# Performance work log

Measured on AMD Instinct MI355X. Metric: run time of the kernel, lower is better.

The kernel has to match this reference:

```python
import jax, jax.numpy as jnp
import numpy as np

B, T, D, H = 128, 512, 64, 512  # batch, seq_len, feature dim, hidden dim
S_MIN, S_FRAC = 0.5, 0.5        # aug_args for generate_samp_mask


def setup_inputs() -> dict:
    key = jax.random.key(0)
    ks = jax.random.split(key, 8)
    x = jax.random.normal(ks[0], (B, T, D), jnp.float32)
    # monotonically increasing irregular timestamps
    tp = jnp.cumsum(jax.random.uniform(ks[1], (B, T), jnp.float32, 1e-3, 0.1), axis=1)
    # Deterministic replay of generate_samp_mask: mask[i]=1 -> teacher forcing
    rng = np.random.default_rng(0)
    extrap_ind = int(rng.integers(int(T * S_MIN), T))
    samp_inds = np.sort(rng.choice(np.arange(extrap_ind), int(S_FRAC * extrap_ind), replace=False))
    mask = np.zeros(T, dtype=np.int32)
    mask[samp_inds] = 1
    samp_mask = jnp.asarray(mask)
    s = 1.0 / np.sqrt(H)  # torch GRUCell/Linear default uniform init scale
    W_ih = jax.random.uniform(ks[2], (3 * H, D + 1), jnp.float32, -s, s)
    W_hh = jax.random.uniform(ks[3], (3 * H, H), jnp.float32, -s, s)
    b_ih = jax.random.uniform(ks[4], (3 * H,), jnp.float32, -s, s)
    b_hh = jax.random.uniform(ks[5], (3 * H,), jnp.float32, -s, s)
    W_out = jax.random.uniform(ks[6], (H, D), jnp.float32, -s, s)
    b_out = jax.random.uniform(ks[7], (D,), jnp.float32, -s, s)
    return {"x": x, "tp": tp, "samp_mask": samp_mask, "W_ih": W_ih, "W_hh": W_hh,
            "b_ih": b_ih, "b_hh": b_hh, "W_out": W_out, "b_out": b_out}


def _gru_cell(inp, h, W_ih, W_hh, b_ih, b_hh):
    gi = inp @ W_ih.T + b_ih          # (B, 3H)
    gh = h @ W_hh.T + b_hh            # (B, 3H)
    i_r, i_z, i_n = jnp.split(gi, 3, axis=-1)
    h_r, h_z, h_n = jnp.split(gh, 3, axis=-1)
    r = jax.nn.sigmoid(i_r + h_r)
    z = jax.nn.sigmoid(i_z + h_z)
    n = jnp.tanh(i_n + r * h_n)
    return (1.0 - z) * n + z * h


def reference(x, tp, samp_mask, W_ih, W_hh, b_ih, b_hh, W_out, b_out):
    # delta_t: append time deltas as an extra channel
    offset = jnp.concatenate([jnp.zeros((tp.shape[0], 1), tp.dtype), tp[:, :-1]], axis=1)
    delta = (tp - offset)[..., None]            # (B, T, 1)
    xin = jnp.concatenate([x, delta], axis=-1)  # (B, T, D+1)

    def step(h, inputs):
        x_t, m = inputs                          # (B, D+1), scalar bool
        prev_out = h @ W_out + b_out             # (B, D)
        ar_in = jnp.concatenate([prev_out, x_t[:, -2:-1]], axis=-1)  # (B, D+1)
        inp = jnp.where(m, x_t, ar_in)
        h_new = _gru_cell(inp, h, W_ih, W_hh, b_ih, b_hh)
        return h_new, h_new

    h0 = jnp.zeros((x.shape[0], H), x.dtype)
    _, h_arr = jax.lax.scan(step, h0, (jnp.swapaxes(xin, 0, 1), samp_mask.astype(bool)))
    h_arr = jnp.swapaxes(h_arr, 0, 1)            # (B, T, H)
    out = h_arr @ W_out + b_out                  # (B, T, D)
    # select_by_length with lens == T for every sample -> flat (B*T, D)
    return out.reshape(-1, out.shape[-1])
```

## Files before the change

### kernel.cpp

```cpp
#include <hip/hip_runtime.h>
#include <math.h>

#define TB 512

typedef __attribute__((ext_vector_type(8))) short bf16x8;
typedef __attribute__((ext_vector_type(4))) float f32x4;
typedef unsigned long long u64;

#define FBASE  24576
#define PREP_F (FBASE)
#define XPRE_F (FBASE + 2112)
#define ORED_F (FBASE + 2904)
#define WOC_F  (FBASE + 3448)
#define WIH_F  (FBASE + 3960)
#define SB_F   (FBASE + 5544)
#define XLAST_F (FBASE + 5640)
#define MSK_F  (FBASE + 5672)
#define LDS_FLOATS (FBASE + 6184)
#define LDS_BYTES (LDS_FLOATS * 4)

#define STEP_BYTES 262144
#define GRP_BYTES  65536
#define HIST_NEEDED (4096ull + 513ull * STEP_BYTES)
#define FB_NEEDED   (4096ull + 2ull * STEP_BYTES)

__device__ __forceinline__ unsigned rne16(float f) {
  unsigned u = __float_as_uint(f);
  return (u + 0x7FFFu + ((u >> 16) & 1u)) >> 16;
}
__device__ __forceinline__ float bfhilo(unsigned hh, unsigned hl) {
  return __uint_as_float(hh << 16) + __uint_as_float(hl << 16);
}

__global__ __launch_bounds__(TB, 2) void gru_persistent(
    const float* __restrict__ x, const float* __restrict__ tp, const int* __restrict__ mask,
    const float* __restrict__ W_ih, const float* __restrict__ W_hh,
    const float* __restrict__ b_ih, const float* __restrict__ b_hh,
    const float* __restrict__ W_out, const float* __restrict__ b_out,
    char* __restrict__ data, unsigned* __restrict__ flags,
    float* __restrict__ out, int hmode)
{
  extern __shared__ char smem[];
  float* LP = (float*)smem;
  int* MSK = (int*)&LP[MSK_F];
  const int tid = threadIdx.x;
  const int wg  = blockIdx.x;
  const int s   = wg & 63;
  const int g   = wg >> 6;
  const int bg0 = g * 32;
  const int j0  = 8 * s;
  const int lane = tid & 63;
  const int wv   = tid >> 6;
  const int myct = wv >> 1, mykh = wv & 1;

  MSK[tid] = mask[tid];
  if (tid < 65) {
    for (int p = 0; p < 24; ++p) {
      int row = (p < 8) ? (j0 + p) : (p < 16) ? (512 + j0 + (p - 8)) : (1024 + j0 + (p - 16));
      LP[WIH_F + p * 66 + tid] = W_ih[(size_t)row * 65 + tid];
    }
  }
  LP[WOC_F + tid] = W_out[(size_t)tid * 64 + s];
  if (tid < 16) {
    int row = (tid < 8) ? (j0 + tid) : (512 + j0 + (tid - 8));
    const float* wi = W_ih + (size_t)row * 65;
    float bt = b_ih[row] + b_hh[row];
    float bp = 0.f;
    for (int d = 0; d < 64; ++d) bp = fmaf(wi[d], b_out[d], bp);
    LP[SB_F + tid]      = bt;
    LP[SB_F + 16 + tid] = bt + bp;
    LP[SB_F + 32 + tid] = wi[64];
  } else if (tid < 24) {
    int jj = tid - 16;
    int row = 1024 + j0 + jj;
    const float* wi = W_ih + (size_t)row * 65;
    float bp = 0.f;
    for (int d = 0; d < 64; ++d) bp = fmaf(wi[d], b_out[d], bp);
    LP[SB_F + 48 + jj] = b_hh[row];
    LP[SB_F + 56 + jj] = b_ih[row];
    LP[SB_F + 64 + jj] = b_ih[row] + bp;
    LP[SB_F + 72 + jj] = wi[64];
  }
  if (tid == 0) LP[SB_F + 80] = b_out[s];
  if (tid < 64) {
    u64* p = (u64*)(data + (size_t)g * GRP_BYTES + (size_t)s * 1024 + tid * 16);
    __hip_atomic_store(p,     0ull, __ATOMIC_RELAXED, __HIP_MEMORY_SCOPE_AGENT);
    __hip_atomic_store(p + 1, 0ull, __ATOMIC_RELAXED, __HIP_MEMORY_SCOPE_AGENT);
  }
  __syncthreads();

  {
    const int k = tid;
    const float* wo = W_out + (size_t)k * 64;
    unsigned short* bw16 = (unsigned short*)smem;
    for (int rr = 0; rr < 48; ++rr) {
      int c, col; float w;
      if (rr < 16) {
        c = 1; col = rr;
        int row = (rr < 8) ? (j0 + rr) : (512 + j0 + rr - 8);
        w = W_hh[(size_t)row * 512 + k];
      } else if (rr < 24) {
        c = 0; col = rr - 16;
        w = W_hh[(size_t)(1024 + j0 + rr - 16) * 512 + k];
      } else {
        int p, whrow;
        if (rr < 32) { c = 0; col = rr - 24 + 8; p = 16 + (rr - 24); whrow = -1; }
        else if (rr < 40) { c = 2; col = rr - 32; p = rr - 32; whrow = j0 + rr - 32; }
        else { c = 2; col = rr - 40 + 8; p = 8 + (rr - 40); whrow = 512 + j0 + rr - 40; }
        const float* wr = &LP[WIH_F + p * 66];
        float a = 0.f;
#pragma unroll 8
        for (int d = 0; d < 64; ++d) a = fmaf(wr[d], wo[d], a);
        w = a + (whrow >= 0 ? W_hh[(size_t)whrow * 512 + k] : 0.f);
      }
      unsigned wh = rne16(w);
      float resid = w - __uint_as_float(wh << 16);
      unsigned wl = rne16(resid);
      int base = c * 32768 + (k >> 5) * 1024 + (col | (((k >> 3) & 3) << 4)) * 16 + (k & 7) * 2;
      bw16[base >> 1] = (unsigned short)wh;
      bw16[(base + 16384) >> 1] = (unsigned short)wl;
    }
  }
  __syncthreads();

  bf16x8 Bh[8], Bl[8];
  if (wv < 6) {
#pragma unroll
    for (int i = 0; i < 8; ++i) {
      Bh[i] = *(const bf16x8*)(smem + myct * 32768 + (mykh * 8 + i) * 1024 + lane * 16);
      Bl[i] = *(const bf16x8*)(smem + myct * 32768 + 16384 + (mykh * 8 + i) * 1024 + lane * 16);
    }
  }

  auto stage_x = [&](int tt) {
    if (tt >= 512) return;
    if (MSK[tt] != 0) {
      for (int task = tid; task < 768; task += TB) {
        const int xr = task >> 5, b = task & 31;
        const float* wrow = &LP[WIH_F + xr * 66];
        size_t ti = (size_t)(bg0 + b) * 512 + tt;
        float del = tp[ti] - (tt > 0 ? tp[ti - 1] : 0.f);
        float xa = wrow[64] * del;
        const float4* x4 = (const float4*)(x + ti * 64);
#pragma unroll
        for (int d4 = 0; d4 < 16; ++d4) {
          float4 xv = x4[d4];
          xa = fmaf(wrow[d4 * 4 + 0], xv.x, xa);
          xa = fmaf(wrow[d4 * 4 + 1], xv.y, xa);
          xa = fmaf(wrow[d4 * 4 + 2], xv.z, xa);
          xa = fmaf(wrow[d4 * 4 + 3], xv.w, xa);
        }
        LP[XPRE_F + xr * 33 + b] = xa;
      }
    } else if (tid < 32) {
      LP[XLAST_F + tid] = x[((size_t)(bg0 + tid) * 512 + tt) * 64 + 63];
    }
  };

  stage_x(0);

  unsigned* myflags = &flags[g * 64];

  asm volatile("s_waitcnt vmcnt(0)" ::: "memory");
  __syncthreads();
  if (tid == 0)
    __hip_atomic_store(&myflags[s], 1u, __ATOMIC_RELAXED, __HIP_MEMORY_SCOPE_AGENT);
  if (wv == 0) {
    int cnt = 0;
    while (true) {
      unsigned v = __hip_atomic_load(&myflags[lane], __ATOMIC_RELAXED, __HIP_MEMORY_SCOPE_AGENT);
      if (__ballot(v < 1u) == 0ull) break;
      __builtin_amdgcn_s_sleep(1);
      if (++cnt > 500000) break;
    }
  }
  __syncthreads();

  const unsigned short* ah16 = (const unsigned short*)smem;

  for (int t = 0; t <= 512; ++t) {
    const bool last = (t == 512);
    const bool teacher = (!last) && (MSK[t] != 0);
    const int csel = teacher ? 1 : 2;

    const char* src = data + (size_t)(hmode ? t : (t & 1)) * STEP_BYTES + (size_t)g * GRP_BYTES;
    uint4 v0[4], v1[4];
    if (hmode) {
#pragma unroll
      for (int i = 0; i < 4; ++i) {
        int c = i * 512 + tid, sg = c >> 6, ln = c & 63;
        v0[i] = *(const uint4*)(src + (size_t)((sg * 2 + 0) * 64 + ln) * 16);
        v1[i] = *(const uint4*)(src + (size_t)((sg * 2 + 1) * 64 + ln) * 16);
      }
    } else {
#pragma unroll
      for (int i = 0; i < 4; ++i) {
        int c = i * 512 + tid, sg = c >> 6, ln = c & 63;
        const u64* p0 = (const u64*)(src + (size_t)((sg * 2 + 0) * 64 + ln) * 16);
        const u64* p1 = (const u64*)(src + (size_t)((sg * 2 + 1) * 64 + ln) * 16);
        u64 a0 = __hip_atomic_load(p0,     __ATOMIC_RELAXED, __HIP_MEMORY_SCOPE_AGENT);
        u64 a1 = __hip_atomic_load(p0 + 1, __ATOMIC_RELAXED, __HIP_MEMORY_SCOPE_AGENT);
        u64 b0 = __hip_atomic_load(p1,     __ATOMIC_RELAXED, __HIP_MEMORY_SCOPE_AGENT);
        u64 b1 = __hip_atomic_load(p1 + 1, __ATOMIC_RELAXED, __HIP_MEMORY_SCOPE_AGENT);
        v0[i] = uint4{(unsigned)a0, (unsigned)(a0 >> 32), (unsigned)a1, (unsigned)(a1 >> 32)};
        v1[i] = uint4{(unsigned)b0, (unsigned)(b0 >> 32), (unsigned)b1, (unsigned)(b1 >> 32)};
      }
    }
#pragma unroll
    for (int i = 0; i < 4; ++i) {
      int c = i * 512 + tid, sg = c >> 6, ln = c & 63;
      *(uint4*)(smem + (size_t)(sg * 1024) + ln * 16)        = v0[i];
      *(uint4*)(smem + (size_t)((32 + sg) * 1024) + ln * 16) = v1[i];
    }
    __syncthreads();

    float hp = 0.f;
    if (tid < 256) {
      const int b = tid & 31, jj = tid >> 5;
      const int ks = s >> 2, half = b >> 4;
      const int ln = (b & 15) | ((s & 3) << 4);
      unsigned hh = ah16[((half * 32 + ks) * 1024 + ln * 16 + jj * 2) >> 1];
      unsigned hl = ah16[((half * 32 + 16 + ks) * 1024 + ln * 16 + jj * 2) >> 1];
      hp = bfhilo(hh, hl);
    }

    if (!last && wv < 6 && (myct == 0 || myct == csel)) {
#pragma unroll
      for (int half = 0; half < 2; ++half) {
        f32x4 acc0 = {0.f, 0.f, 0.f, 0.f};
        f32x4 acc1 = {0.f, 0.f, 0.f, 0.f};
        f32x4 acc2 = {0.f, 0.f, 0.f, 0.f};
        f32x4 acc3 = {0.f, 0.f, 0.f, 0.f};
#pragma unroll
        for (int i = 0; i < 8; ++i) {
          const char* abh = smem + (size_t)((half * 32 + mykh * 8 + i) * 1024) + lane * 16;
          bf16x8 ahh = *(const bf16x8*)abh;
          bf16x8 ahl = *(const bf16x8*)(abh + 16 * 1024);
          f32x4& acc = ((i & 3) == 0) ? acc0 : ((i & 3) == 1) ? acc1 : ((i & 3) == 2) ? acc2 : acc3;
          acc = __builtin_amdgcn_mfma_f32_16x16x32_bf16(ahh, Bh[i], acc, 0, 0, 0);
          acc = __builtin_amdgcn_mfma_f32_16x16x32_bf16(ahh, Bl[i], acc, 0, 0, 0);
          acc = __builtin_amdgcn_mfma_f32_16x16x32_bf16(ahl, Bh[i], acc, 0, 0, 0);
        }
        f32x4 acc = (acc0 + acc1) + (acc2 + acc3);
        const int prow = (myct == 0 ? 16 : 0) + (lane & 15);
        const int pcol = half * 16 + ((lane >> 4) << 2);
#pragma unroll
        for (int q = 0; q < 4; ++q)
          LP[PREP_F + mykh * 1056 + prow * 33 + pcol + q] = acc[q];
      }
    }

    if (wv >= 6) {
#pragma unroll
      for (int tk = 0; tk < 4; ++tk) {
        const int task = (tid - 384) + tk * 128;
        const int half = task >> 8, rem = task & 255;
        const int bl = rem & 15, ks = rem >> 4;
        const int b = half * 16 + bl;
        const float* woc = &LP[WOC_F];
        float oa = 0.f;
#pragma unroll
        for (int c = 0; c < 4; ++c) {
          const uint4 wh = *(const uint4*)(smem + (size_t)((half * 32 + ks) * 1024) + (bl | (c << 4)) * 16);
          const uint4 wl = *(const uint4*)(smem + (size_t)((half * 32 + 16 + ks) * 1024) + (bl | (c << 4)) * 16);
          int k0 = ks * 32 + c * 8;
          oa = fmaf(bfhilo(wh.x & 0xFFFFu, wl.x & 0xFFFFu), woc[k0 + 0], oa);
          oa = fmaf(bfhilo(wh.x >> 16, wl.x >> 16), woc[k0 + 1], oa);
          oa = fmaf(bfhilo(wh.y & 0xFFFFu, wl.y & 0xFFFFu), woc[k0 + 2], oa);
          oa = fmaf(bfhilo(wh.y >> 16, wl.y >> 16), woc[k0 + 3], oa);
          oa = fmaf(bfhilo(wh.z & 0xFFFFu, wl.z & 0xFFFFu), woc[k0 + 4], oa);
          oa = fmaf(bfhilo(wh.z >> 16, wl.z >> 16), woc[k0 + 5], oa);
          oa = fmaf(bfhilo(wh.w & 0xFFFFu, wl.w & 0xFFFFu), woc[k0 + 6], oa);
          oa = fmaf(bfhilo(wh.w >> 16, wl.w >> 16), woc[k0 + 7], oa);
        }
        LP[ORED_F + b * 17 + ks] = oa;
      }
    }
    __syncthreads();

    if (!last) {
      if (tid < 256) {
        const int b = tid & 31, jj = tid >> 5;
        float pr  = LP[PREP_F + jj * 33 + b]        + LP[PREP_F + 1056 + jj * 33 + b];
        float pz  = LP[PREP_F + (8 + jj) * 33 + b]  + LP[PREP_F + 1056 + (8 + jj) * 33 + b];
        float pnh = LP[PREP_F + (16 + jj) * 33 + b] + LP[PREP_F + 1056 + (16 + jj) * 33 + b]
                  + LP[SB_F + 48 + jj];
        float pni;
        if (teacher) {
          pr += LP[XPRE_F + jj * 33 + b] + LP[SB_F + jj];
          pz += LP[XPRE_F + (8 + jj) * 33 + b] + LP[SB_F + 8 + jj];
          pni = LP[XPRE_F + (16 + jj) * 33 + b] + LP[SB_F + 56 + jj];
        } else {
          float xl = LP[XLAST_F + b];
          pr += LP[SB_F + 16 + jj] + LP[SB_F + 32 + jj] * xl;
          pz += LP[SB_F + 24 + jj] + LP[SB_F + 40 + jj] * xl;
          pni = LP[PREP_F + (24 + jj) * 33 + b] + LP[PREP_F + 1056 + (24 + jj) * 33 + b]
              + LP[SB_F + 64 + jj] + LP[SB_F + 72 + jj] * xl;
        }
        float rg = 1.f / (1.f + expf(-pr));
        float zg = 1.f / (1.f + expf(-pz));
        float ng = tanhf(fmaf(rg, pnh, pni));
        float hv = fmaf(zg, hp - ng, ng);
        float hvp = __shfl_xor(hv, 32, 64);
        if ((jj & 1) == 0) {
          unsigned h0h = rne16(hv), h1h = rne16(hvp);
          float r0 = hv  - __uint_as_float(h0h << 16);
          float r1 = hvp - __uint_as_float(h1h << 16);
          unsigned hw = h0h | (h1h << 16);
          unsigned lw = rne16(r0) | (rne16(r1) << 16);
          char* dst = data + (size_t)(hmode ? (t + 1) : ((t + 1) & 1)) * STEP_BYTES
                    + (size_t)g * GRP_BYTES;
          const int half = b >> 4, ln2 = (b & 15) | ((s & 3) << 4), ks2 = s >> 2;
          unsigned* dhh = (unsigned*)(dst + (size_t)((ks2 * 2 + half) * 64 + ln2) * 16 + jj * 2);
          unsigned* dhl = (unsigned*)(dst + (size_t)(((16 + ks2) * 2 + half) * 64 + ln2) * 16 + jj * 2);
          __hip_atomic_store(dhh, hw, __ATOMIC_RELAXED, __HIP_MEMORY_SCOPE_AGENT);
          __hip_atomic_store(dhl, lw, __ATOMIC_RELAXED, __HIP_MEMORY_SCOPE_AGENT);
        }
      }
      asm volatile("s_waitcnt vmcnt(0)" ::: "memory");
      __syncthreads();
      const unsigned tgt = (unsigned)(t + 2);
      if (tid == 0)
        __hip_atomic_store(&myflags[s], tgt, __ATOMIC_RELAXED, __HIP_MEMORY_SCOPE_AGENT);
      if (t >= 1 && tid >= 256 && tid < 288) {
        const int b = tid - 256;
        float o = LP[SB_F + 80];
#pragma unroll
        for (int i = 0; i < 16; ++i) o += LP[ORED_F + b * 17 + i];
        out[((size_t)(bg0 + b) * 512 + (t - 1)) * 64 + s] = o;
      }
      stage_x(t + 1);
      if (wv == 0) {
        int cnt = 0;
        while (true) {
          unsigned v = __hip_atomic_load(&myflags[lane], __ATOMIC_RELAXED, __HIP_MEMORY_SCOPE_AGENT);
          if (__ballot(v < tgt) == 0ull) break;
          __builtin_amdgcn_s_sleep(1);
          if (++cnt > 200000) break;
        }
      }
      __syncthreads();
    } else {
      if (tid >= 256 && tid < 288) {
        const int b = tid - 256;
        float o = LP[SB_F + 80];
#pragma unroll
        for (int i = 0; i < 16; ++i) o += LP[ORED_F + b * 17 + i];
        out[((size_t)(bg0 + b) * 512 + 511) * 64 + s] = o;
      }
    }
  }
}

extern "C" void kernel_launch(void* const* d_in, const int* in_sizes, int n_in,
                              void* d_out, int out_size, void* d_ws, size_t ws_size,
                              hipStream_t stream) {
  (void)in_sizes; (void)n_in; (void)out_size;
  const float* x    = (const float*)d_in[0];
  const float* tp   = (const float*)d_in[1];
  const int*   mask = (const int*)d_in[2];
  const float* W_ih = (const float*)d_in[3];
  const float* W_hh = (const float*)d_in[4];
  const float* b_ih = (const float*)d_in[5];
  const float* b_hh = (const float*)d_in[6];
  const float* W_out= (const float*)d_in[7];
  const float* b_out= (const float*)d_in[8];
  float* out = (float*)d_out;
  if (ws_size < FB_NEEDED) return;
  int hmode = (ws_size >= HIST_NEEDED) ? 1 : 0;
  unsigned* flags = (unsigned*)d_ws;
  char* dataptr = (char*)d_ws + 4096;
  hipMemsetAsync(flags, 0, 4096, stream);
  hipFuncSetAttribute((const void*)gru_persistent,
                      hipFuncAttributeMaxDynamicSharedMemorySize, LDS_BYTES);
  hipLaunchKernelGGL(gru_persistent, dim3(256), dim3(TB), LDS_BYTES, stream,
                     x, tp, mask, W_ih, W_hh, b_ih, b_hh, W_out, b_out, dataptr, flags, out, hmode);
}
```

Before: 3.396 ms.

## Pin GRU batch groups to XCDs and double workgroup count with halved batch tiles

New measurement: 6.269 ms. 1.85x slower.

```diff
diff --git a/kernel.cpp b/kernel.cpp
--- a/kernel.cpp
+++ b/kernel.cpp
@@ -2,27 +2,29 @@
 #include <math.h>
 
 #define TB 512
+#define NWG 512
 
 typedef __attribute__((ext_vector_type(8))) short bf16x8;
 typedef __attribute__((ext_vector_type(4))) float f32x4;
 typedef unsigned long long u64;
 
-#define FBASE  24576
-#define PREP_F (FBASE)
-#define XPRE_F (FBASE + 2112)
-#define ORED_F (FBASE + 2904)
-#define WOC_F  (FBASE + 3448)
-#define WIH_F  (FBASE + 3960)
-#define SB_F   (FBASE + 5544)
-#define XLAST_F (FBASE + 5640)
-#define MSK_F  (FBASE + 5672)
-#define LDS_FLOATS (FBASE + 6184)
+#define PREP_F 8192
+#define XPRE_F 9280
+#define ORED_F 9688
+#define WOC_F  9960
+#define WIH_F  10472
+#define SB_F   12056
+#define XLAST_F 12152
+#define MSK_F  12168
+#define ROLE_F 12680
+#define LDS_FLOATS 12688
 #define LDS_BYTES (LDS_FLOATS * 4)
 
-#define STEP_BYTES 262144
-#define GRP_BYTES  65536
-#define HIST_NEEDED (4096ull + 513ull * STEP_BYTES)
-#define FB_NEEDED   (4096ull + 2ull * STEP_BYTES)
+#define GRP_BYTES 32768
+#define STEP_BYTES (8 * GRP_BYTES)
+#define DATA_OFF 4096
+#define HIST_NEEDED ((unsigned long long)DATA_OFF + 513ull * STEP_BYTES)
+#define FB_NEEDED   ((unsigned long long)DATA_OFF + 2ull * STEP_BYTES)
 
 __device__ __forceinline__ unsigned rne16(float f) {
   unsigned u = __float_as_uint(f);
@@ -32,26 +34,51 @@
   return __uint_as_float(hh << 16) + __uint_as_float(hl << 16);
 }
 
-__global__ __launch_bounds__(TB, 2) void gru_persistent(
+__global__ __launch_bounds__(TB, 4) void gru_persistent(
     const float* __restrict__ x, const float* __restrict__ tp, const int* __restrict__ mask,
     const float* __restrict__ W_ih, const float* __restrict__ W_hh,
     const float* __restrict__ b_ih, const float* __restrict__ b_hh,
     const float* __restrict__ W_out, const float* __restrict__ b_out,
-    char* __restrict__ data, unsigned* __restrict__ flags,
-    float* __restrict__ out, int hmode)
+    char* __restrict__ ws, float* __restrict__ out, int hist)
 {
   extern __shared__ char smem[];
   float* LP = (float*)smem;
   int* MSK = (int*)&LP[MSK_F];
+  volatile int* ROLE = (volatile int*)&LP[ROLE_F];
   const int tid = threadIdx.x;
-  const int wg  = blockIdx.x;
-  const int s   = wg & 63;
-  const int g   = wg >> 6;
-  const int bg0 = g * 32;
-  const int j0  = 8 * s;
   const int lane = tid & 63;
   const int wv   = tid >> 6;
   const int myct = wv >> 1, mykh = wv & 1;
+
+  unsigned* flags = (unsigned*)ws;
+  unsigned* reg   = (unsigned*)(ws + 2048);
+  char* data = ws + DATA_OFF;
+
+  if (tid == 0) {
+    unsigned xcc = 0;
+    asm volatile("s_getreg_b32 %0, hwreg(HW_REG_XCC_ID)" : "=s"(xcc));
+    xcc &= 7u;
+    unsigned rank = __hip_atomic_fetch_add(&reg[xcc], 1u, __ATOMIC_RELAXED, __HIP_MEMORY_SCOPE_AGENT);
+    __hip_atomic_fetch_add(&reg[8], 1u, __ATOMIC_RELAXED, __HIP_MEMORY_SCOPE_AGENT);
+    int cnt = 0;
+    while (__hip_atomic_load(&reg[8], __ATOMIC_RELAXED, __HIP_MEMORY_SCOPE_AGENT) < (unsigned)NWG) {
+      __builtin_amdgcn_s_sleep(8);
+      if (++cnt > 2000000) break;
+    }
+    int ok = 1;
+    for (int i = 0; i < 8; ++i)
+      ok &= (__hip_atomic_load(&reg[i], __ATOMIC_RELAXED, __HIP_MEMORY_SCOPE_AGENT) == 64u);
+    ok &= (rank < 64u);
+    ROLE[0] = ok ? (int)xcc : (int)(blockIdx.x & 7);
+    ROLE[1] = ok ? (int)rank : (int)(blockIdx.x >> 3);
+    ROLE[2] = ok;
+  }
+  __syncthreads();
+  const int g = ROLE[0];
+  const int s = ROLE[1];
+  const int mode = (ROLE[2] && hist) ? 2 : (hist ? 1 : 0);
+  const int bg0 = g * 16;
+  const int j0  = 8 * s;
 
   MSK[tid] = mask[tid];
   if (tid < 65) {
@@ -82,61 +109,72 @@
     LP[SB_F + 72 + jj] = wi[64];
   }
   if (tid == 0) LP[SB_F + 80] = b_out[s];
-  if (tid < 64) {
-    u64* p = (u64*)(data + (size_t)g * GRP_BYTES + (size_t)s * 1024 + tid * 16);
-    __hip_atomic_store(p,     0ull, __ATOMIC_RELAXED, __HIP_MEMORY_SCOPE_AGENT);
-    __hip_atomic_store(p + 1, 0ull, __ATOMIC_RELAXED, __HIP_MEMORY_SCOPE_AGENT);
-  }
   __syncthreads();
 
+  bf16x8 Bh[8], Bl[8];
   {
-    const int k = tid;
-    const float* wo = W_out + (size_t)k * 64;
     unsigned short* bw16 = (unsigned short*)smem;
-    for (int rr = 0; rr < 48; ++rr) {
-      int c, col; float w;
-      if (rr < 16) {
-        c = 1; col = rr;
-        int row = (rr < 8) ? (j0 + rr) : (512 + j0 + rr - 8);
-        w = W_hh[(size_t)row * 512 + k];
-      } else if (rr < 24) {
-        c = 0; col = rr - 16;
-        w = W_hh[(size_t)(1024 + j0 + rr - 16) * 512 + k];
-      } else {
-        int p, whrow;
-        if (rr < 32) { c = 0; col = rr - 24 + 8; p = 16 + (rr - 24); whrow = -1; }
-        else if (rr < 40) { c = 2; col = rr - 32; p = rr - 32; whrow = j0 + rr - 32; }
-        else { c = 2; col = rr - 40 + 8; p = 8 + (rr - 40); whrow = 512 + j0 + rr - 40; }
-        const float* wr = &LP[WIH_F + p * 66];
-        float a = 0.f;
+    for (int ct = 0; ct < 3; ++ct) {
+      const int k = tid;
+      const float* wo = W_out + (size_t)k * 64;
+      for (int wr = 0; wr < 16; ++wr) {
+        float w;
+        if (ct == 1) {
+          int row = (wr < 8) ? (j0 + wr) : (512 + j0 + wr - 8);
+          w = W_hh[(size_t)row * 512 + k];
+        } else if (ct == 0) {
+          if (wr < 8) w = W_hh[(size_t)(1024 + j0 + wr) * 512 + k];
+          else {
+            const float* wrp = &LP[WIH_F + (16 + wr - 8) * 66];
+            float a = 0.f;
 #pragma unroll 8
-        for (int d = 0; d < 64; ++d) a = fmaf(wr[d], wo[d], a);
-        w = a + (whrow >= 0 ? W_hh[(size_t)whrow * 512 + k] : 0.f);
-      }
-      unsigned wh = rne16(w);
-      float resid = w - __uint_as_float(wh << 16);
-      unsigned wl = rne16(resid);
-      int base = c * 32768 + (k >> 5) * 1024 + (col | (((k >> 3) & 3) << 4)) * 16 + (k & 7) * 2;
-      bw16[base >> 1] = (unsigned short)wh;
-      bw16[(base + 16384) >> 1] = (unsigned short)wl;
-    }
-  }
-  __syncthreads();
-
-  bf16x8 Bh[8], Bl[8];
-  if (wv < 6) {
-#pragma unroll
-    for (int i = 0; i < 8; ++i) {
-      Bh[i] = *(const bf16x8*)(smem + myct * 32768 + (mykh * 8 + i) * 1024 + lane * 16);
-      Bl[i] = *(const bf16x8*)(smem + myct * 32768 + 16384 + (mykh * 8 + i) * 1024 + lane * 16);
+            for (int d = 0; d < 64; ++d) a = fmaf(wrp[d], wo[d], a);
+            w = a;
+          }
+        } else {
+          int row = (wr < 8) ? (j0 + wr) : (512 + j0 + wr - 8);
+          const float* wrp = &LP[WIH_F + wr * 66];
+          float a = 0.f;
+#pragma unroll 8
+          for (int d = 0; d < 64; ++d) a = fmaf(wrp[d], wo[d], a);
+          w = a + W_hh[(size_t)row * 512 + k];
+        }
+        unsigned wh = rne16(w);
+        float resid = w - __uint_as_float(wh << 16);
+        unsigned wl = rne16(resid);
+        int base = (k >> 5) * 1024 + (wr | (((k >> 3) & 3) << 4)) * 16 + (k & 7) * 2;
+        bw16[base >> 1] = (unsigned short)wh;
+        bw16[(base + 16384) >> 1] = (unsigned short)wl;
+      }
+      __syncthreads();
+      if (wv < 6 && myct == ct) {
+#pragma unroll
+        for (int i = 0; i < 8; ++i) {
+          Bh[i] = *(const bf16x8*)(smem + (mykh * 8 + i) * 1024 + lane * 16);
+          Bl[i] = *(const bf16x8*)(smem + 16384 + (mykh * 8 + i) * 1024 + lane * 16);
+        }
+      }
+      __syncthreads();
+    }
+  }
+
+  if (tid < 32) {
+    const int b = tid & 15, term = tid >> 4;
+    size_t off = (size_t)(term * 16 + (s >> 2)) * 1024 + (size_t)(b | ((s & 3) << 4)) * 16;
+    u64* p = (u64*)(data + (size_t)g * GRP_BYTES + off);
+    if (mode == 2) {
+      *(volatile u64*)p = 0ull; *(volatile u64*)(p + 1) = 0ull;
+    } else {
+      __hip_atomic_store(p,     0ull, __ATOMIC_RELAXED, __HIP_MEMORY_SCOPE_AGENT);
+      __hip_atomic_store(p + 1, 0ull, __ATOMIC_RELAXED, __HIP_MEMORY_SCOPE_AGENT);
     }
   }
 
   auto stage_x = [&](int tt) {
     if (tt >= 512) return;
     if (MSK[tt] != 0) {
-      for (int task = tid; task < 768; task += TB) {
-        const int xr = task >> 5, b = task & 31;
+      if (tid < 384) {
+        const int xr = tid >> 4, b = tid & 15;
         const float* wrow = &LP[WIH_F + xr * 66];
         size_t ti = (size_t)(bg0 + b) * 512 + tt;
         float del = tp[ti] - (tt > 0 ? tp[ti - 1] : 0.f);
@@ -150,30 +188,40 @@
           xa = fmaf(wrow[d4 * 4 + 2], xv.z, xa);
           xa = fmaf(wrow[d4 * 4 + 3], xv.w, xa);
         }
-        LP[XPRE_F + xr * 33 + b] = xa;
-      }
-    } else if (tid < 32) {
+        LP[XPRE_F + xr * 17 + b] = xa;
+      }
+    } else if (tid < 16) {
       LP[XLAST_F + tid] = x[((size_t)(bg0 + tid) * 512 + tt) * 64 + 63];
     }
   };
 
+  unsigned* myflags = &flags[g * 64];
+  auto flag_put = [&](unsigned tgt) {
+    if (mode == 2)
+      __hip_atomic_fetch_add(&myflags[s], 1u, __ATOMIC_RELAXED, __HIP_MEMORY_SCOPE_WORKGROUP);
+    else
+      __hip_atomic_store(&myflags[s], tgt, __ATOMIC_RELAXED, __HIP_MEMORY_SCOPE_AGENT);
+  };
+  auto flag_poll = [&](unsigned tgt) {
+    int cnt = 0;
+    while (true) {
+      unsigned v;
+      if (mode == 2)
+        v = __hip_atomic_fetch_add(&myflags[lane], 0x10000u, __ATOMIC_RELAXED,
+                                   __HIP_MEMORY_SCOPE_WORKGROUP) & 0xFFFFu;
+      else
+        v = __hip_atomic_load(&myflags[lane], __ATOMIC_RELAXED, __HIP_MEMORY_SCOPE_AGENT);
+      if (__ballot(v < tgt) == 0ull) break;
+      __builtin_amdgcn_s_sleep(1);
+      if (++cnt > 500000) break;
+    }
+  };
+
   stage_x(0);
-
-  unsigned* myflags = &flags[g * 64];
-
   asm volatile("s_waitcnt vmcnt(0)" ::: "memory");
   __syncthreads();
-  if (tid == 0)
-    __hip_atomic_store(&myflags[s], 1u, __ATOMIC_RELAXED, __HIP_MEMORY_SCOPE_AGENT);
-  if (wv == 0) {
-    int cnt = 0;
-    while (true) {
-      unsigned v = __hip_atomic_load(&myflags[lane], __ATOMIC_RELAXED, __HIP_MEMORY_SCOPE_AGENT);
-      if (__ballot(v < 1u) == 0ull) break;
-      __builtin_amdgcn_s_sleep(1);
-      if (++cnt > 500000) break;
-    }
-  }
+  if (tid == 0) flag_put(1u);
+  if (wv == 7) flag_poll(1u);
   __syncthreads();
 
   const unsigned short* ah16 = (const unsigned short*)smem;
@@ -182,87 +230,65 @@
     const bool last = (t == 512);
     const bool teacher = (!last) && (MSK[t] != 0);
     const int csel = teacher ? 1 : 2;
-
-    const char* src = data + (size_t)(hmode ? t : (t & 1)) * STEP_BYTES + (size_t)g * GRP_BYTES;
-    uint4 v0[4], v1[4];
-    if (hmode) {
+    const char* src = data + (size_t)(hist ? t : (t & 1)) * STEP_BYTES + (size_t)g * GRP_BYTES;
+
+    if (mode == 0) {
+      u64 a0[4], a1[4];
 #pragma unroll
       for (int i = 0; i < 4; ++i) {
-        int c = i * 512 + tid, sg = c >> 6, ln = c & 63;
-        v0[i] = *(const uint4*)(src + (size_t)((sg * 2 + 0) * 64 + ln) * 16);
-        v1[i] = *(const uint4*)(src + (size_t)((sg * 2 + 1) * 64 + ln) * 16);
+        const u64* p = (const u64*)(src + (size_t)(i * 512 + tid) * 16);
+        a0[i] = __hip_atomic_load(p,     __ATOMIC_RELAXED, __HIP_MEMORY_SCOPE_AGENT);
+        a1[i] = __hip_atomic_load(p + 1, __ATOMIC_RELAXED, __HIP_MEMORY_SCOPE_AGENT);
+      }
+#pragma unroll
+      for (int i = 0; i < 4; ++i) {
+        u64* d = (u64*)(smem + (size_t)(i * 512 + tid) * 16);
+        d[0] = a0[i]; d[1] = a1[i];
       }
     } else {
-#pragma unroll
-      for (int i = 0; i < 4; ++i) {
-        int c = i * 512 + tid, sg = c >> 6, ln = c & 63;
-        const u64* p0 = (const u64*)(src + (size_t)((sg * 2 + 0) * 64 + ln) * 16);
-        const u64* p1 = (const u64*)(src + (size_t)((sg * 2 + 1) * 64 + ln) * 16);
-        u64 a0 = __hip_atomic_load(p0,     __ATOMIC_RELAXED, __HIP_MEMORY_SCOPE_AGENT);
-        u64 a1 = __hip_atomic_load(p0 + 1, __ATOMIC_RELAXED, __HIP_MEMORY_SCOPE_AGENT);
-        u64 b0 = __hip_atomic_load(p1,     __ATOMIC_RELAXED, __HIP_MEMORY_SCOPE_AGENT);
-        u64 b1 = __hip_atomic_load(p1 + 1, __ATOMIC_RELAXED, __HIP_MEMORY_SCOPE_AGENT);
-        v0[i] = uint4{(unsigned)a0, (unsigned)(a0 >> 32), (unsigned)a1, (unsigned)(a1 >> 32)};
-        v1[i] = uint4{(unsigned)b0, (unsigned)(b0 >> 32), (unsigned)b1, (unsigned)(b1 >> 32)};
-      }
-    }
-#pragma unroll
-    for (int i = 0; i < 4; ++i) {
-      int c = i * 512 + tid, sg = c >> 6, ln = c & 63;
-      *(uint4*)(smem + (size_t)(sg * 1024) + ln * 16)        = v0[i];
-      *(uint4*)(smem + (size_t)((32 + sg) * 1024) + ln * 16) = v1[i];
+      uint4 v[4];
+#pragma unroll
+      for (int i = 0; i < 4; ++i) v[i] = *(const uint4*)(src + (size_t)(i * 512 + tid) * 16);
+#pragma unroll
+      for (int i = 0; i < 4; ++i) *(uint4*)(smem + (size_t)(i * 512 + tid) * 16) = v[i];
     }
     __syncthreads();
 
-    float hp = 0.f;
-    if (tid < 256) {
-      const int b = tid & 31, jj = tid >> 5;
-      const int ks = s >> 2, half = b >> 4;
-      const int ln = (b & 15) | ((s & 3) << 4);
-      unsigned hh = ah16[((half * 32 + ks) * 1024 + ln * 16 + jj * 2) >> 1];
-      unsigned hl = ah16[((half * 32 + 16 + ks) * 1024 + ln * 16 + jj * 2) >> 1];
-      hp = bfhilo(hh, hl);
-    }
-
     if (!last && wv < 6 && (myct == 0 || myct == csel)) {
-#pragma unroll
-      for (int half = 0; half < 2; ++half) {
-        f32x4 acc0 = {0.f, 0.f, 0.f, 0.f};
-        f32x4 acc1 = {0.f, 0.f, 0.f, 0.f};
-        f32x4 acc2 = {0.f, 0.f, 0.f, 0.f};
-        f32x4 acc3 = {0.f, 0.f, 0.f, 0.f};
-#pragma unroll
-        for (int i = 0; i < 8; ++i) {
-          const char* abh = smem + (size_t)((half * 32 + mykh * 8 + i) * 1024) + lane * 16;
-          bf16x8 ahh = *(const bf16x8*)abh;
-          bf16x8 ahl = *(const bf16x8*)(abh + 16 * 1024);
-          f32x4& acc = ((i & 3) == 0) ? acc0 : ((i & 3) == 1) ? acc1 : ((i & 3) == 2) ? acc2 : acc3;
-          acc = __builtin_amdgcn_mfma_f32_16x16x32_bf16(ahh, Bh[i], acc, 0, 0, 0);
-          acc = __builtin_amdgcn_mfma_f32_16x16x32_bf16(ahh, Bl[i], acc, 0, 0, 0);
-          acc = __builtin_amdgcn_mfma_f32_16x16x32_bf16(ahl, Bh[i], acc, 0, 0, 0);
-        }
-        f32x4 acc = (acc0 + acc1) + (acc2 + acc3);
-        const int prow = (myct == 0 ? 16 : 0) + (lane & 15);
-        const int pcol = half * 16 + ((lane >> 4) << 2);
-#pragma unroll
-        for (int q = 0; q < 4; ++q)
-          LP[PREP_F + mykh * 1056 + prow * 33 + pcol + q] = acc[q];
-      }
+      f32x4 acc0 = {0.f, 0.f, 0.f, 0.f};
+      f32x4 acc1 = {0.f, 0.f, 0.f, 0.f};
+      f32x4 acc2 = {0.f, 0.f, 0.f, 0.f};
+      f32x4 acc3 = {0.f, 0.f, 0.f, 0.f};
+#pragma unroll
+      for (int i = 0; i < 8; ++i) {
+        const char* abh = smem + (size_t)((mykh * 8 + i) * 1024) + lane * 16;
+        bf16x8 ahh = *(const bf16x8*)abh;
+        bf16x8 ahl = *(const bf16x8*)(abh + 16384);
+        f32x4& acc = ((i & 3) == 0) ? acc0 : ((i & 3) == 1) ? acc1 : ((i & 3) == 2) ? acc2 : acc3;
+        acc = __builtin_amdgcn_mfma_f32_16x16x32_bf16(ahh, Bh[i], acc, 0, 0, 0);
+        acc = __builtin_amdgcn_mfma_f32_16x16x32_bf16(ahh, Bl[i], acc, 0, 0, 0);
+        acc = __builtin_amdgcn_mfma_f32_16x16x32_bf16(ahl, Bh[i], acc, 0, 0, 0);
+      }
+      f32x4 acc = (acc0 + acc1) + (acc2 + acc3);
+      const int slot = (myct == 0) ? 0 : 1;
+      const int prow = lane & 15;
+      const int bcol = (lane >> 4) << 2;
+#pragma unroll
+      for (int q = 0; q < 4; ++q)
+        LP[PREP_F + (mykh * 2 + slot) * 272 + prow * 17 + bcol + q] = acc[q];
     }
 
     if (wv >= 6) {
 #pragma unroll
-      for (int tk = 0; tk < 4; ++tk) {
+      for (int tk = 0; tk < 2; ++tk) {
         const int task = (tid - 384) + tk * 128;
-        const int half = task >> 8, rem = task & 255;
-        const int bl = rem & 15, ks = rem >> 4;
-        const int b = half * 16 + bl;
+        const int b = task & 15, ks = task >> 4;
         const float* woc = &LP[WOC_F];
         float oa = 0.f;
 #pragma unroll
         for (int c = 0; c < 4; ++c) {
-          const uint4 wh = *(const uint4*)(smem + (size_t)((half * 32 + ks) * 1024) + (bl | (c << 4)) * 16);
-          const uint4 wl = *(const uint4*)(smem + (size_t)((half * 32 + 16 + ks) * 1024) + (bl | (c << 4)) * 16);
+          const uint4 wh = *(const uint4*)(smem + (size_t)(ks * 1024) + (b | (c << 4)) * 16);
+          const uint4 wl = *(const uint4*)(smem + (size_t)(16384 + ks * 1024) + (b | (c << 4)) * 16);
           int k0 = ks * 32 + c * 8;
           oa = fmaf(bfhilo(wh.x & 0xFFFFu, wl.x & 0xFFFFu), woc[k0 + 0], oa);
           oa = fmaf(bfhilo(wh.x >> 16, wl.x >> 16), woc[k0 + 1], oa);
@@ -279,50 +305,55 @@
     __syncthreads();
 
     if (!last) {
-      if (tid < 256) {
-        const int b = tid & 31, jj = tid >> 5;
-        float pr  = LP[PREP_F + jj * 33 + b]        + LP[PREP_F + 1056 + jj * 33 + b];
-        float pz  = LP[PREP_F + (8 + jj) * 33 + b]  + LP[PREP_F + 1056 + (8 + jj) * 33 + b];
-        float pnh = LP[PREP_F + (16 + jj) * 33 + b] + LP[PREP_F + 1056 + (16 + jj) * 33 + b]
+      if (tid < 128) {
+        const int b = tid & 15, jj = tid >> 4;
+        float pr  = LP[PREP_F + 1 * 272 + jj * 17 + b] + LP[PREP_F + 3 * 272 + jj * 17 + b];
+        float pz  = LP[PREP_F + 1 * 272 + (8 + jj) * 17 + b] + LP[PREP_F + 3 * 272 + (8 + jj) * 17 + b];
+        float pnh = LP[PREP_F + 0 * 272 + jj * 17 + b] + LP[PREP_F + 2 * 272 + jj * 17 + b]
                   + LP[SB_F + 48 + jj];
         float pni;
         if (teacher) {
-          pr += LP[XPRE_F + jj * 33 + b] + LP[SB_F + jj];
-          pz += LP[XPRE_F + (8 + jj) * 33 + b] + LP[SB_F + 8 + jj];
-          pni = LP[XPRE_F + (16 + jj) * 33 + b] + LP[SB_F + 56 + jj];
+          pr += LP[XPRE_F + jj * 17 + b] + LP[SB_F + jj];
+          pz += LP[XPRE_F + (8 + jj) * 17 + b] + LP[SB_F + 8 + jj];
+          pni = LP[XPRE_F + (16 + jj) * 17 + b] + LP[SB_F + 56 + jj];
         } else {
           float xl = LP[XLAST_F + b];
           pr += LP[SB_F + 16 + jj] + LP[SB_F + 32 + jj] * xl;
           pz += LP[SB_F + 24 + jj] + LP[SB_F + 40 + jj] * xl;
-          pni = LP[PREP_F + (24 + jj) * 33 + b] + LP[PREP_F + 1056 + (24 + jj) * 33 + b]
+          pni = LP[PREP_F + 0 * 272 + (8 + jj) * 17 + b] + LP[PREP_F + 2 * 272 + (8 + jj) * 17 + b]
               + LP[SB_F + 64 + jj] + LP[SB_F + 72 + jj] * xl;
         }
+        size_t hoff = (size_t)(s >> 2) * 1024 + (size_t)(b | ((s & 3) << 4)) * 16 + (size_t)jj * 2;
+        float hp = bfhilo(ah16[hoff >> 1], ah16[(hoff + 16384) >> 1]);
         float rg = 1.f / (1.f + expf(-pr));
         float zg = 1.f / (1.f + expf(-pz));
         float ng = tanhf(fmaf(rg, pnh, pni));
         float hv = fmaf(zg, hp - ng, ng);
-        float hvp = __shfl_xor(hv, 32, 64);
+        float hvp = __shfl_xor(hv, 16, 64);
         if ((jj & 1) == 0) {
           unsigned h0h = rne16(hv), h1h = rne16(hvp);
           float r0 = hv  - __uint_as_float(h0h << 16);
           float r1 = hvp - __uint_as_float(h1h << 16);
           unsigned hw = h0h | (h1h << 16);
           unsigned lw = rne16(r0) | (rne16(r1) << 16);
-          char* dst = data + (size_t)(hmode ? (t + 1) : ((t + 1) & 1)) * STEP_BYTES
+          char* dst = data + (size_t)(hist ? (t + 1) : ((t + 1) & 1)) * STEP_BYTES
                     + (size_t)g * GRP_BYTES;
-          const int half = b >> 4, ln2 = (b & 15) | ((s & 3) << 4), ks2 = s >> 2;
-          unsigned* dhh = (unsigned*)(dst + (size_t)((ks2 * 2 + half) * 64 + ln2) * 16 + jj * 2);
-          unsigned* dhl = (unsigned*)(dst + (size_t)(((16 + ks2) * 2 + half) * 64 + ln2) * 16 + jj * 2);
-          __hip_atomic_store(dhh, hw, __ATOMIC_RELAXED, __HIP_MEMORY_SCOPE_AGENT);
-          __hip_atomic_store(dhl, lw, __ATOMIC_RELAXED, __HIP_MEMORY_SCOPE_AGENT);
+          unsigned* dhh = (unsigned*)(dst + hoff);
+          unsigned* dhl = (unsigned*)(dst + 16384 + hoff);
+          if (mode == 2) {
+            *(volatile unsigned*)dhh = hw;
+            *(volatile unsigned*)dhl = lw;
+          } else {
+            __hip_atomic_store(dhh, hw, __ATOMIC_RELAXED, __HIP_MEMORY_SCOPE_AGENT);
+            __hip_atomic_store(dhl, lw, __ATOMIC_RELAXED, __HIP_MEMORY_SCOPE_AGENT);
+          }
         }
       }
       asm volatile("s_waitcnt vmcnt(0)" ::: "memory");
       __syncthreads();
       const unsigned tgt = (unsigned)(t + 2);
-      if (tid == 0)
-        __hip_atomic_store(&myflags[s], tgt, __ATOMIC_RELAXED, __HIP_MEMORY_SCOPE_AGENT);
-      if (t >= 1 && tid >= 256 && tid < 288) {
+      if (tid == 0) flag_put(tgt);
+      if (t >= 1 && tid >= 256 && tid < 272) {
         const int b = tid - 256;
         float o = LP[SB_F + 80];
 #pragma unroll
@@ -330,18 +361,10 @@
         out[((size_t)(bg0 + b) * 512 + (t - 1)) * 64 + s] = o;
       }
       stage_x(t + 1);
-      if (wv == 0) {
-        int cnt = 0;
-        while (true) {
-          unsigned v = __hip_atomic_load(&myflags[lane], __ATOMIC_RELAXED, __HIP_MEMORY_SCOPE_AGENT);
-          if (__ballot(v < tgt) == 0ull) break;
-          __builtin_amdgcn_s_sleep(1);
-          if (++cnt > 200000) break;
-        }
-      }
+      if (wv == 7) flag_poll(tgt);
       __syncthreads();
     } else {
-      if (tid >= 256 && tid < 288) {
+      if (tid >= 256 && tid < 272) {
         const int b = tid - 256;
         float o = LP[SB_F + 80];
 #pragma unroll
@@ -367,12 +390,11 @@
   const float* b_out= (const float*)d_in[8];
   float* out = (float*)d_out;
   if (ws_size < FB_NEEDED) return;
-  int hmode = (ws_size >= HIST_NEEDED) ? 1 : 0;
-  unsigned* flags = (unsigned*)d_ws;
-  char* dataptr = (char*)d_ws + 4096;
-  hipMemsetAsync(flags, 0, 4096, stream);
+  int hist = (ws_size >= HIST_NEEDED) ? 1 : 0;
+  hipMemsetAsync(d_ws, 0, 4096, stream);
   hipFuncSetAttribute((const void*)gru_persistent,
                       hipFuncAttributeMaxDynamicSharedMemorySize, LDS_BYTES);
-  hipLaunchKernelGGL(gru_persistent, dim3(256), dim3(TB), LDS_BYTES, stream,
-                     x, tp, mask, W_ih, W_hh, b_ih, b_hh, W_out, b_out, dataptr, flags, out, hmode);
+  hipLaunchKernelGGL(gru_persistent, dim3(NWG), dim3(TB), LDS_BYTES, stream,
+                     x, tp, mask, W_ih, W_hh, b_ih, b_hh, W_out, b_out,
+                     (char*)d_ws, out, hist);
 }
```
